# Kernel tuning notes

Measured on AMD Instinct MI355X. Metric: run time of the kernel, lower is better.

## Reference

```python
import jax, jax.numpy as jnp
import numpy as np

NUM_ITEMS = 100000
HIDDEN = 128
NNZ = 1600000


def setup_inputs() -> dict:
    key = jax.random.key(0)
    k1, k2, k3, k4, k5, k6 = jax.random.split(key, 6)
    item_embedding_table = jax.random.normal(k1, (NUM_ITEMS, HIDDEN), dtype=jnp.float32)
    adj_rows = jnp.sort(jax.random.randint(k2, (NNZ,), 0, NUM_ITEMS, dtype=jnp.int32))
    adj_cols = jax.random.randint(k3, (NNZ,), 0, NUM_ITEMS, dtype=jnp.int32)
    adj_vals = jax.random.uniform(k4, (NNZ,), dtype=jnp.float32)
    # nn.Linear default init (uniform in +-1/sqrt(fan_in)) approximated by scaled normal
    W_weight = jax.random.normal(k5, (HIDDEN, HIDDEN), dtype=jnp.float32) / np.sqrt(HIDDEN)
    W_bias = jax.random.normal(k6, (HIDDEN,), dtype=jnp.float32) * 0.01
    return {
        "item_embedding_table": item_embedding_table,
        "adj_rows": adj_rows,
        "adj_cols": adj_cols,
        "adj_vals": adj_vals,
        "W_weight": W_weight,
        "W_bias": W_bias,
    }


def reference(item_embedding_table, adj_rows, adj_cols, adj_vals, W_weight, W_bias):
    # support = W(x): x @ W^T + b   (nn.Linear convention: weight [out, in])
    support = jnp.einsum("nd,hd->nh", item_embedding_table, W_weight) + W_bias  # [N, H]
    # output = sparse_coo(adj) @ support, via gather + segment-sum scatter
    msgs = adj_vals[:, None] * support[adj_cols]  # [nnz, H]
    output = jax.ops.segment_sum(msgs, adj_rows, num_segments=NUM_ITEMS)  # [N, H]
    return output
```

## Files before the change

### kernel.cpp

```cpp
#include <hip/hip_runtime.h>
#include <hip/hip_fp16.h>

#define N_ITEMS 100000
#define HID 128
#define NNZ_T 1600000
#define RP_BLOCKS 391
#define GEMM_TILES 1563
#define GEMM_BLOCKS 781
#define SPMM_BLOCKS 12500

typedef unsigned short ushort_t;
typedef unsigned int uint_t;
typedef short bf16x8 __attribute__((ext_vector_type(8)));
typedef float f32x4 __attribute__((ext_vector_type(4)));
typedef float f32x4v __attribute__((ext_vector_type(4)));
typedef uint_t u32x4v __attribute__((ext_vector_type(4)));

static __device__ __forceinline__ ushort_t f32_to_bf16(float f) {
    uint_t u = __float_as_uint(f);
    uint_t r = (u + 0x7FFFu + ((u >> 16) & 1u)) >> 16;
    return (ushort_t)r;
}

static __device__ __forceinline__ __half2 u2h2(uint_t w) {
    union { uint_t u; __half2 h; } c; c.u = w; return c.h;
}

__global__ __launch_bounds__(256) void prep_gemm(
    const float* __restrict__ X, const float* __restrict__ W,
    const float* __restrict__ bias, const int* __restrict__ rows,
    ushort_t* __restrict__ S, int* __restrict__ row_ptr) {
    if (blockIdx.x < RP_BLOCKS) {
        int r = blockIdx.x * 256 + threadIdx.x;
        if (r > N_ITEMS) return;
        int lo = 0, hi = NNZ_T;
        while (lo < hi) {
            int mid = (lo + hi) >> 1;
            if (rows[mid] < r) lo = mid + 1; else hi = mid;
        }
        row_ptr[r] = lo;
        return;
    }

    __shared__ ushort_t Wl[HID * HID];
    {
        const int t = threadIdx.x;
        const float4* Wf = (const float4*)W;
#pragma unroll
        for (int j = 0; j < 8; ++j) {
            const int gblk = j * 256 + t;
            float4 w0 = Wf[gblk * 2];
            float4 w1 = Wf[gblk * 2 + 1];
            bf16x8 v;
            v[0] = (short)f32_to_bf16(w0.x); v[1] = (short)f32_to_bf16(w0.y);
            v[2] = (short)f32_to_bf16(w0.z); v[3] = (short)f32_to_bf16(w0.w);
            v[4] = (short)f32_to_bf16(w1.x); v[5] = (short)f32_to_bf16(w1.y);
            v[6] = (short)f32_to_bf16(w1.z); v[7] = (short)f32_to_bf16(w1.w);
            const int ps = (gblk * 8) ^ (((gblk >> 4) & 7) << 3);
            *(bf16x8*)&Wl[ps] = v;
        }
    }
    __syncthreads();

    const int lane = threadIdx.x & 63;
    const int wave = threadIdx.x >> 6;
    const int m = lane & 15;
    const int q = lane >> 4;
    const int swz = (m & 7) << 3;

    for (int tile = blockIdx.x - RP_BLOCKS; tile < GEMM_TILES; tile += GEMM_BLOCKS) {
        const int row0 = tile * 64 + wave * 16;
        int arow = row0 + m;
        if (arow >= N_ITEMS) arow = N_ITEMS - 1;

        f32x4 acc[8] = {};
#pragma unroll
        for (int kb = 0; kb < 4; ++kb) {
            const int k0 = kb * 32 + q * 8;
            f32x4v a0 = __builtin_nontemporal_load((const f32x4v*)&X[(size_t)arow * HID + k0]);
            f32x4v a1 = __builtin_nontemporal_load((const f32x4v*)&X[(size_t)arow * HID + k0 + 4]);
            bf16x8 xf;
            xf[0] = (short)f32_to_bf16(a0[0]); xf[1] = (short)f32_to_bf16(a0[1]);
            xf[2] = (short)f32_to_bf16(a0[2]); xf[3] = (short)f32_to_bf16(a0[3]);
            xf[4] = (short)f32_to_bf16(a1[0]); xf[5] = (short)f32_to_bf16(a1[1]);
            xf[6] = (short)f32_to_bf16(a1[2]); xf[7] = (short)f32_to_bf16(a1[3]);
#pragma unroll
            for (int nt = 0; nt < 8; ++nt) {
                const bf16x8 wf = *(const bf16x8*)&Wl[((nt * 16 + m) * HID + k0) ^ swz];
                acc[nt] = __builtin_amdgcn_mfma_f32_16x16x32_bf16(wf, xf, acc[nt], 0, 0, 0);
            }
        }

        const int srow = row0 + m;
        const bool ok = srow < N_ITEMS;
#pragma unroll
        for (int nt = 0; nt < 8; ++nt) {
            const int c0 = nt * 16 + q * 4;
            float4 bv = *(const float4*)&bias[c0];
            ushort_t h0 = __half_as_ushort(__float2half(acc[nt][0] + bv.x));
            ushort_t h1 = __half_as_ushort(__float2half(acc[nt][1] + bv.y));
            ushort_t h2 = __half_as_ushort(__float2half(acc[nt][2] + bv.z));
            ushort_t h3 = __half_as_ushort(__float2half(acc[nt][3] + bv.w));
            uint2 pk;
            pk.x = (uint_t)h0 | ((uint_t)h1 << 16);
            pk.y = (uint_t)h2 | ((uint_t)h3 << 16);
            if (ok) *(uint2*)&S[(size_t)srow * HID + c0] = pk;
        }
    }
}

__global__ __launch_bounds__(256) void spmm_csr(
    const int* __restrict__ cols, const float* __restrict__ vals,
    const int* __restrict__ row_ptr, const ushort_t* __restrict__ S,
    float* __restrict__ out) {
    const int lane = threadIdx.x & 63;
    const int wid = blockIdx.x * 4 + ((threadIdx.x >> 6) & 3);
    const int r0 = wid * 2;
    if (r0 >= N_ITEMS) return;

    const int g = lane >> 4;
    const int l = lane & 15;
    const int sel = lane >> 5;

    const int2 p01 = *(const int2*)&row_ptr[r0];
    const int pEb = row_ptr[r0 + 2];
    int pa = p01.x; const int pEa = p01.y;
    int pb = p01.y;

    __half2 accA[4], accB[4];
#pragma unroll
    for (int j = 0; j < 4; ++j) { accA[j] = __float2half2_rn(0.f); accB[j] = __float2half2_rn(0.f); }

    while (pa < pEa || pb < pEb) {
        const int base = sel ? pb : pa;
        const int end  = sel ? pEb : pEa;
        const int idx  = base + (lane & 15);
        const int cidx = max(min(idx, end - 1), 0);
        const int c_l  = cols[cidx];
        const float v_l = (idx < end) ? vals[cidx] : 0.f;

        u32x4v uA[4], uB[4];
        float vA[4], vB[4];
#pragma unroll
        for (int t = 0; t < 4; ++t) {
            const int sa = 4 * t + g;
            const int ca = __shfl(c_l, sa, 64);
            vA[t] = __shfl(v_l, sa, 64);
            uA[t] = __builtin_nontemporal_load((const u32x4v*)&S[(size_t)ca * HID + 8 * l]);
            const int cb = __shfl(c_l, 32 + sa, 64);
            vB[t] = __shfl(v_l, 32 + sa, 64);
            uB[t] = __builtin_nontemporal_load((const u32x4v*)&S[(size_t)cb * HID + 8 * l]);
        }
#pragma unroll
        for (int t = 0; t < 4; ++t) {
            const __half2 wa = __float2half2_rn(vA[t]);
            accA[0] = __hfma2(wa, u2h2(uA[t][0]), accA[0]);
            accA[1] = __hfma2(wa, u2h2(uA[t][1]), accA[1]);
            accA[2] = __hfma2(wa, u2h2(uA[t][2]), accA[2]);
            accA[3] = __hfma2(wa, u2h2(uA[t][3]), accA[3]);
            const __half2 wb = __float2half2_rn(vB[t]);
            accB[0] = __hfma2(wb, u2h2(uB[t][0]), accB[0]);
            accB[1] = __hfma2(wb, u2h2(uB[t][1]), accB[1]);
            accB[2] = __hfma2(wb, u2h2(uB[t][2]), accB[2]);
            accB[3] = __hfma2(wb, u2h2(uB[t][3]), accB[3]);
        }
        pa = min(pa + 16, pEa);
        pb = min(pb + 16, pEb);
    }

    float fA[8], fB[8];
#pragma unroll
    for (int j = 0; j < 4; ++j) {
        fA[2 * j] = __low2float(accA[j]);  fA[2 * j + 1] = __high2float(accA[j]);
        fB[2 * j] = __low2float(accB[j]);  fB[2 * j + 1] = __high2float(accB[j]);
    }
#pragma unroll
    for (int e = 0; e < 8; ++e) {
        fA[e] += __shfl_xor(fA[e], 16, 64);
        fA[e] += __shfl_xor(fA[e], 32, 64);
        fB[e] += __shfl_xor(fB[e], 16, 64);
        fB[e] += __shfl_xor(fB[e], 32, 64);
    }
    if (g == 0) {
        float* p = &out[(size_t)r0 * HID + 8 * l];
        f32x4v o0; o0[0] = fA[0]; o0[1] = fA[1]; o0[2] = fA[2]; o0[3] = fA[3];
        f32x4v o1; o1[0] = fA[4]; o1[1] = fA[5]; o1[2] = fA[6]; o1[3] = fA[7];
        __builtin_nontemporal_store(o0, (f32x4v*)p);
        __builtin_nontemporal_store(o1, (f32x4v*)(p + 4));
    } else if (g == 1 && r0 + 1 < N_ITEMS) {
        float* p = &out[(size_t)(r0 + 1) * HID + 8 * l];
        f32x4v o0; o0[0] = fB[0]; o0[1] = fB[1]; o0[2] = fB[2]; o0[3] = fB[3];
        f32x4v o1; o1[0] = fB[4]; o1[1] = fB[5]; o1[2] = fB[6]; o1[3] = fB[7];
        __builtin_nontemporal_store(o0, (f32x4v*)p);
        __builtin_nontemporal_store(o1, (f32x4v*)(p + 4));
    }
}

extern "C" void kernel_launch(void* const* d_in, const int* in_sizes, int n_in,
                              void* d_out, int out_size, void* d_ws, size_t ws_size,
                              hipStream_t stream) {
    const float* X    = (const float*)d_in[0];
    const int*   rows = (const int*)  d_in[1];
    const int*   cols = (const int*)  d_in[2];
    const float* vals = (const float*)d_in[3];
    const float* W    = (const float*)d_in[4];
    const float* bias = (const float*)d_in[5];
    float* out = (float*)d_out;

    ushort_t* S       = (ushort_t*)d_ws;
    int*      row_ptr = (int*)(S + (size_t)N_ITEMS * HID);

    prep_gemm<<<RP_BLOCKS + GEMM_BLOCKS, 256, 0, stream>>>(X, W, bias, rows, S, row_ptr);
    spmm_csr<<<SPMM_BLOCKS, 256, 0, stream>>>(cols, vals, row_ptr, S, out);
}
```

Baseline: 208.1 us.

## Process one CSR row per wave in SpMM and drop nontemporal hints

The SpMM kernel now assigns a single output row to each wave instead of two rows split across half-waves, and doubles the grid accordingly. Nontemporal loads and stores are replaced by ordinary cached accesses in both kernels, and the row-pointer binary-search blocks are placed after the GEMM blocks in the fused prep launch. This simplifies the inner loop but halves the gathers in flight per wave and may leave lanes idle on short rows.

```diff
diff --git a/kernel.cpp b/kernel.cpp
--- a/kernel.cpp
+++ b/kernel.cpp
@@ -4,17 +4,15 @@
 #define N_ITEMS 100000
 #define HID 128
 #define NNZ_T 1600000
-#define RP_BLOCKS 391
 #define GEMM_TILES 1563
 #define GEMM_BLOCKS 781
-#define SPMM_BLOCKS 12500
+#define RP_BLOCKS 391
+#define SPMM_BLOCKS 25000
 
 typedef unsigned short ushort_t;
 typedef unsigned int uint_t;
 typedef short bf16x8 __attribute__((ext_vector_type(8)));
 typedef float f32x4 __attribute__((ext_vector_type(4)));
-typedef float f32x4v __attribute__((ext_vector_type(4)));
-typedef uint_t u32x4v __attribute__((ext_vector_type(4)));
 
 static __device__ __forceinline__ ushort_t f32_to_bf16(float f) {
     uint_t u = __float_as_uint(f);
@@ -22,16 +20,12 @@
     return (ushort_t)r;
 }
 
-static __device__ __forceinline__ __half2 u2h2(uint_t w) {
-    union { uint_t u; __half2 h; } c; c.u = w; return c.h;
-}
-
 __global__ __launch_bounds__(256) void prep_gemm(
     const float* __restrict__ X, const float* __restrict__ W,
     const float* __restrict__ bias, const int* __restrict__ rows,
     ushort_t* __restrict__ S, int* __restrict__ row_ptr) {
-    if (blockIdx.x < RP_BLOCKS) {
-        int r = blockIdx.x * 256 + threadIdx.x;
+    if (blockIdx.x >= GEMM_BLOCKS) {
+        int r = (blockIdx.x - GEMM_BLOCKS) * 256 + threadIdx.x;
         if (r > N_ITEMS) return;
         int lo = 0, hi = NNZ_T;
         while (lo < hi) {
@@ -68,7 +62,7 @@
     const int q = lane >> 4;
     const int swz = (m & 7) << 3;
 
-    for (int tile = blockIdx.x - RP_BLOCKS; tile < GEMM_TILES; tile += GEMM_BLOCKS) {
+    for (int tile = blockIdx.x; tile < GEMM_TILES; tile += GEMM_BLOCKS) {
         const int row0 = tile * 64 + wave * 16;
         int arow = row0 + m;
         if (arow >= N_ITEMS) arow = N_ITEMS - 1;
@@ -77,13 +71,13 @@
 #pragma unroll
         for (int kb = 0; kb < 4; ++kb) {
             const int k0 = kb * 32 + q * 8;
-            f32x4v a0 = __builtin_nontemporal_load((const f32x4v*)&X[(size_t)arow * HID + k0]);
-            f32x4v a1 = __builtin_nontemporal_load((const f32x4v*)&X[(size_t)arow * HID + k0 + 4]);
+            float4 a0 = *(const float4*)&X[(size_t)arow * HID + k0];
+            float4 a1 = *(const float4*)&X[(size_t)arow * HID + k0 + 4];
             bf16x8 xf;
-            xf[0] = (short)f32_to_bf16(a0[0]); xf[1] = (short)f32_to_bf16(a0[1]);
-            xf[2] = (short)f32_to_bf16(a0[2]); xf[3] = (short)f32_to_bf16(a0[3]);
-            xf[4] = (short)f32_to_bf16(a1[0]); xf[5] = (short)f32_to_bf16(a1[1]);
-            xf[6] = (short)f32_to_bf16(a1[2]); xf[7] = (short)f32_to_bf16(a1[3]);
+            xf[0] = (short)f32_to_bf16(a0.x); xf[1] = (short)f32_to_bf16(a0.y);
+            xf[2] = (short)f32_to_bf16(a0.z); xf[3] = (short)f32_to_bf16(a0.w);
+            xf[4] = (short)f32_to_bf16(a1.x); xf[5] = (short)f32_to_bf16(a1.y);
+            xf[6] = (short)f32_to_bf16(a1.z); xf[7] = (short)f32_to_bf16(a1.w);
 #pragma unroll
             for (int nt = 0; nt < 8; ++nt) {
                 const bf16x8 wf = *(const bf16x8*)&Wl[((nt * 16 + m) * HID + k0) ^ swz];
@@ -114,85 +108,59 @@
     const int* __restrict__ row_ptr, const ushort_t* __restrict__ S,
     float* __restrict__ out) {
     const int lane = threadIdx.x & 63;
-    const int wid = blockIdx.x * 4 + ((threadIdx.x >> 6) & 3);
-    const int r0 = wid * 2;
-    if (r0 >= N_ITEMS) return;
+    const int r = blockIdx.x * 4 + (threadIdx.x >> 6);
+    if (r >= N_ITEMS) return;
 
     const int g = lane >> 4;
     const int l = lane & 15;
-    const int sel = lane >> 5;
 
-    const int2 p01 = *(const int2*)&row_ptr[r0];
-    const int pEb = row_ptr[r0 + 2];
-    int pa = p01.x; const int pEa = p01.y;
-    int pb = p01.y;
+    int pa = row_ptr[r];
+    const int pE = row_ptr[r + 1];
 
-    __half2 accA[4], accB[4];
+    __half2 acc[4];
 #pragma unroll
-    for (int j = 0; j < 4; ++j) { accA[j] = __float2half2_rn(0.f); accB[j] = __float2half2_rn(0.f); }
+    for (int j = 0; j < 4; ++j) acc[j] = __float2half2_rn(0.f);
 
-    while (pa < pEa || pb < pEb) {
-        const int base = sel ? pb : pa;
-        const int end  = sel ? pEb : pEa;
-        const int idx  = base + (lane & 15);
-        const int cidx = max(min(idx, end - 1), 0);
+    while (pa < pE) {
+        const int idx  = pa + l;
+        const int cidx = min(idx, pE - 1);
         const int c_l  = cols[cidx];
-        const float v_l = (idx < end) ? vals[cidx] : 0.f;
+        const float v_l = (idx < pE) ? vals[cidx] : 0.f;
 
-        u32x4v uA[4], uB[4];
-        float vA[4], vB[4];
+        uint4 u[4];
+        float vv[4];
 #pragma unroll
         for (int t = 0; t < 4; ++t) {
-            const int sa = 4 * t + g;
-            const int ca = __shfl(c_l, sa, 64);
-            vA[t] = __shfl(v_l, sa, 64);
-            uA[t] = __builtin_nontemporal_load((const u32x4v*)&S[(size_t)ca * HID + 8 * l]);
-            const int cb = __shfl(c_l, 32 + sa, 64);
-            vB[t] = __shfl(v_l, 32 + sa, 64);
-            uB[t] = __builtin_nontemporal_load((const u32x4v*)&S[(size_t)cb * HID + 8 * l]);
+            const int s = 4 * t + g;
+            const int ct = __shfl(c_l, s, 64);
+            vv[t] = __shfl(v_l, s, 64);
+            u[t] = *(const uint4*)&S[(size_t)ct * HID + 8 * l];
         }
 #pragma unroll
         for (int t = 0; t < 4; ++t) {
-            const __half2 wa = __float2half2_rn(vA[t]);
-            accA[0] = __hfma2(wa, u2h2(uA[t][0]), accA[0]);
-            accA[1] = __hfma2(wa, u2h2(uA[t][1]), accA[1]);
-            accA[2] = __hfma2(wa, u2h2(uA[t][2]), accA[2]);
-            accA[3] = __hfma2(wa, u2h2(uA[t][3]), accA[3]);
-            const __half2 wb = __float2half2_rn(vB[t]);
-            accB[0] = __hfma2(wb, u2h2(uB[t][0]), accB[0]);
-            accB[1] = __hfma2(wb, u2h2(uB[t][1]), accB[1]);
-            accB[2] = __hfma2(wb, u2h2(uB[t][2]), accB[2]);
-            accB[3] = __hfma2(wb, u2h2(uB[t][3]), accB[3]);
+            const __half2 w = __float2half2_rn(vv[t]);
+            acc[0] = __hfma2(w, *(const __half2*)&u[t].x, acc[0]);
+            acc[1] = __hfma2(w, *(const __half2*)&u[t].y, acc[1]);
+            acc[2] = __hfma2(w, *(const __half2*)&u[t].z, acc[2]);
+            acc[3] = __hfma2(w, *(const __half2*)&u[t].w, acc[3]);
         }
-        pa = min(pa + 16, pEa);
-        pb = min(pb + 16, pEb);
+        pa += 16;
     }
 
-    float fA[8], fB[8];
+    float f[8];
 #pragma unroll
     for (int j = 0; j < 4; ++j) {
-        fA[2 * j] = __low2float(accA[j]);  fA[2 * j + 1] = __high2float(accA[j]);
-        fB[2 * j] = __low2float(accB[j]);  fB[2 * j + 1] = __high2float(accB[j]);
+        f[2 * j] = __low2float(acc[j]);  f[2 * j + 1] = __high2float(acc[j]);
     }
 #pragma unroll
     for (int e = 0; e < 8; ++e) {
-        fA[e] += __shfl_xor(fA[e], 16, 64);
-        fA[e] += __shfl_xor(fA[e], 32, 64);
-        fB[e] += __shfl_xor(fB[e], 16, 64);
-        fB[e] += __shfl_xor(fB[e], 32, 64);
+        f[e] += __shfl_xor(f[e], 16, 64);
+        f[e] += __shfl_xor(f[e], 32, 64);
     }
     if (g == 0) {
-        float* p = &out[(size_t)r0 * HID + 8 * l];
-        f32x4v o0; o0[0] = fA[0]; o0[1] = fA[1]; o0[2] = fA[2]; o0[3] = fA[3];
-        f32x4v o1; o1[0] = fA[4]; o1[1] = fA[5]; o1[2] = fA[6]; o1[3] = fA[7];
-        __builtin_nontemporal_store(o0, (f32x4v*)p);
-        __builtin_nontemporal_store(o1, (f32x4v*)(p + 4));
-    } else if (g == 1 && r0 + 1 < N_ITEMS) {
-        float* p = &out[(size_t)(r0 + 1) * HID + 8 * l];
-        f32x4v o0; o0[0] = fB[0]; o0[1] = fB[1]; o0[2] = fB[2]; o0[3] = fB[3];
-        f32x4v o1; o1[0] = fB[4]; o1[1] = fB[5]; o1[2] = fB[6]; o1[3] = fB[7];
-        __builtin_nontemporal_store(o0, (f32x4v*)p);
-        __builtin_nontemporal_store(o1, (f32x4v*)(p + 4));
+        float* p = &out[(size_t)r * HID + 8 * l];
+        *(float4*)p       = make_float4(f[0], f[1], f[2], f[3]);
+        *(float4*)(p + 4) = make_float4(f[4], f[5], f[6], f[7]);
     }
 }
 
@@ -210,6 +178,6 @@
     ushort_t* S       = (ushort_t*)d_ws;
     int*      row_ptr = (int*)(S + (size_t)N_ITEMS * HID);
 
-    prep_gemm<<<RP_BLOCKS + GEMM_BLOCKS, 256, 0, stream>>>(X, W, bias, rows, S, row_ptr);
+    prep_gemm<<<GEMM_BLOCKS + RP_BLOCKS, 256, 0, stream>>>(X, W, bias, rows, S, row_ptr);
     spmm_csr<<<SPMM_BLOCKS, 256, 0, stream>>>(cols, vals, row_ptr, S, out);
 }
```

Result: faster. 188.6 us (median of 2 runs) (-9.4%).
